# Performance work log

Measured on AMD Instinct MI355X. Metric: run time of the kernel, lower is better.

Reference implementation:

```python
import jax, jax.numpy as jnp
import numpy as np

B, N, C, H = 32, 577, 768, 12

def setup_inputs() -> dict:
    key = jax.random.key(0)
    k1, k2, k3, k4 = jax.random.split(key, 4)
    x = jax.random.normal(k1, (B, N, C), dtype=jnp.float32)
    prev = jax.random.normal(k2, (B, H, N, N), dtype=jnp.float32)
    Wqkv = jax.random.normal(k3, (3 * C, C), dtype=jnp.float32) * (C ** -0.5)
    Wproj = jax.random.normal(k4, (C, C), dtype=jnp.float32) * (C ** -0.5)
    bproj = jnp.zeros((C,), dtype=jnp.float32)
    return {"x": x, "prev": prev, "Wqkv": Wqkv, "Wproj": Wproj, "bproj": bproj}

def reference(x, prev, Wqkv, Wproj, bproj):
    b, n, c = x.shape
    h = H
    hd = c // h
    scale = hd ** -0.5
    # qkv: [B, N, 3C] -> [3, B, H, N, hd]
    qkv = (x @ Wqkv.T).reshape(b, n, 3, h, hd).transpose(2, 0, 3, 1, 4)
    q, k, v = qkv[0], qkv[1], qkv[2]
    # pre-softmax scores with residual passthrough (res_score=True)
    scores = jnp.einsum('bhqd,bhkd->bhqk', q, k) * scale + prev
    attn = jax.nn.softmax(scores, axis=-1)
    out = jnp.einsum('bhqk,bhkd->bhqd', attn, v)  # [B, H, N, hd]
    out = out.transpose(0, 2, 1, 3).reshape(b, n, c)
    out = out @ Wproj.T + bproj
    return out, scores
```

## Files before the change

kernel.cpp:

```cpp
#include <hip/hip_runtime.h>
#include <cstdint>
#include <cstddef>

using short8   = __attribute__((ext_vector_type(8))) short;
using f32x4    = __attribute__((ext_vector_type(4))) float;
using ushort4v = __attribute__((ext_vector_type(4))) unsigned short;

#define B_    32
#define N_    577
#define C_    768
#define H_    12
#define HD_   64
#define NPAD  640
#define MROWS 18464
#define MPAD  18560
#define NQKV  2304
#define SCALE 0.125f
#define OUT0_ELTS 14180352

static __device__ __forceinline__ unsigned short f2bf(float f) {
  union { float f; unsigned int u; } v; v.f = f;
  return (unsigned short)((v.u + 0x7FFFu + ((v.u >> 16) & 1u)) >> 16);
}

static __device__ __forceinline__ void gload_lds16(const unsigned short* g, unsigned short* l) {
  __builtin_amdgcn_global_load_lds(
      (const __attribute__((address_space(1))) unsigned int*)g,
      (__attribute__((address_space(3))) unsigned int*)l, 16, 0, 0);
}

__global__ __launch_bounds__(256) void cvt_f32_bf16(const float* __restrict__ src,
                                                    unsigned short* __restrict__ dst, int n4) {
  int i = blockIdx.x * 256 + threadIdx.x;
  if (i >= n4) return;
  f32x4 v = ((const f32x4*)src)[i];
  ushort4v o;
  o.x = f2bf(v.x); o.y = f2bf(v.y); o.z = f2bf(v.z); o.w = f2bf(v.w);
  ((ushort4v*)dst)[i] = o;
}

__global__ __launch_bounds__(256) void gemm_qkv(
    const unsigned short* __restrict__ A,
    const unsigned short* __restrict__ Bw,
    unsigned short* __restrict__ qb,
    unsigned short* __restrict__ kbuf,
    unsigned short* __restrict__ vtb)
{
  __shared__ union {
    struct { unsigned short A[128 * 64]; unsigned short B[128 * 64]; } st;
    unsigned short ct[128 * 128];
  } lds;
  const int mt = blockIdx.x, nt = blockIdx.y;
  const int tid = threadIdx.x;
  const int wave = tid >> 6, lane = tid & 63;
  const int wm = wave >> 1, wn = wave & 1;
  const int lq = lane & 15, grp = lane >> 4;

  f32x4 acc[4][4] = {};

  const int arowbase = mt * 128;
  const int browbase = nt * 128;
  const int srow = wave * 8 + (lane >> 3);
  const int scol = (lane & 7) * 8;

  for (int kblk = 0; kblk < 12; ++kblk) {
    const int koff = kblk * 64;
#pragma unroll
    for (int i = 0; i < 4; ++i) {
      gload_lds16(A  + (size_t)(arowbase + i * 32 + srow) * 768 + koff + scol,
                  &lds.st.A[(i * 32 + wave * 8) * 64]);
      gload_lds16(Bw + (size_t)(browbase + i * 32 + srow) * 768 + koff + scol,
                  &lds.st.B[(i * 32 + wave * 8) * 64]);
    }
    __syncthreads();
#pragma unroll
    for (int ks = 0; ks < 2; ++ks) {
      short8 af[4], bf[4];
#pragma unroll
      for (int mi = 0; mi < 4; ++mi)
        af[mi] = *(const short8*)&lds.st.A[(wm * 64 + mi * 16 + lq) * 64 + ks * 32 + grp * 8];
#pragma unroll
      for (int ni = 0; ni < 4; ++ni)
        bf[ni] = *(const short8*)&lds.st.B[(wn * 64 + ni * 16 + lq) * 64 + ks * 32 + grp * 8];
#pragma unroll
      for (int mi = 0; mi < 4; ++mi)
#pragma unroll
        for (int ni = 0; ni < 4; ++ni)
          acc[mi][ni] = __builtin_amdgcn_mfma_f32_16x16x32_bf16(af[mi], bf[ni], acc[mi][ni], 0, 0, 0);
    }
    __syncthreads();
  }

  const int s = nt / 6;

  if (s < 2) {
#pragma unroll
    for (int mi = 0; mi < 4; ++mi)
#pragma unroll
      for (int ni = 0; ni < 4; ++ni) {
        const int col = wn * 64 + ni * 16 + lq;
#pragma unroll
        for (int j = 0; j < 4; ++j) {
          const int row = wm * 64 + mi * 16 + grp * 4 + j;
          const int slot = (col >> 3) ^ (row & 7);
          lds.ct[row * 128 + slot * 8 + (col & 7)] = f2bf(acc[mi][ni][j]);
        }
      }
    __syncthreads();
    unsigned short* dstbase = (s == 0) ? qb : kbuf;
    const int h0 = (nt - s * 6) * 2;
#pragma unroll
    for (int p = 0; p < 4; ++p) {
      const int r  = p * 32 + (tid >> 3);
      const int cp = tid & 7;
      const int m  = arowbase + r;
      const unsigned bb = (unsigned)m / 577u;
      const int t = m - (int)bb * 577;
      const bool valid = (m < MROWS);
      const int cpos = cp ^ (t & 7);
#pragma unroll
      for (int hh = 0; hh < 2; ++hh) {
        const int slot = ((hh * 8 + cp) ^ (r & 7));
        short8 val = *(const short8*)&lds.ct[r * 128 + slot * 8];
        if (valid) {
          unsigned short* dst = dstbase +
              (((size_t)(bb * H_ + h0 + hh) * NPAD + t) * HD_ + cpos * 8);
          *(short8*)dst = val;
        }
      }
    }
  } else {
#pragma unroll
    for (int mi = 0; mi < 4; ++mi) {
#pragma unroll
      for (int ni = 0; ni < 4; ++ni) {
        const int n = browbase + wn * 64 + ni * 16 + lq;
        const int rem = n - 1536;
        const int hh = rem >> 6, d = rem & 63;
#pragma unroll
        for (int j = 0; j < 4; ++j) {
          const int m = arowbase + wm * 64 + mi * 16 + grp * 4 + j;
          if (m < MROWS) {
            const unsigned bb = (unsigned)m / 577u;
            const int t = m - (int)bb * 577;
            const int tloc = t & 63;
            const int newcol = (t & ~63) + ((((tloc >> 3) ^ (d & 7)) << 3)) + (t & 7);
            vtb[((size_t)bb * H_ + hh) * HD_ * NPAD + (size_t)d * NPAD + newcol] =
                f2bf(acc[mi][ni][j]);
          }
        }
      }
    }
  }
}

__global__ __launch_bounds__(256, 3) void attn_kernel(
    const unsigned short* __restrict__ qb,
    const unsigned short* __restrict__ kb,
    const unsigned short* __restrict__ vtb,
    const float* __restrict__ prev,
    float* __restrict__ scores_out,
    unsigned short* __restrict__ ob)
{
  const int qblk = blockIdx.x;
  const int bh   = blockIdx.y;
  const int tid  = threadIdx.x;
  const int wave = tid >> 6;
  const int lane = tid & 63;
  const int lq = lane & 15, grp = lane >> 4;

  const int b = bh / H_;
  const int h = bh - b * H_;

  const unsigned short* qp = qb  + (size_t)bh * NPAD * HD_;
  const unsigned short* kp = kb  + (size_t)bh * NPAD * HD_;
  const unsigned short* vp = vtb + (size_t)bh * HD_ * NPAD;

  const int qrow = qblk * 64 + wave * 16 + lq;
  const bool qvalid = (qrow < N_);
  const bool counted = (qblk < 9);

  const float* prevrow_c = prev + ((size_t)bh * N_ + (qvalid ? qrow : (N_ - 1))) * N_;
  const float* prevbh = prev + (size_t)bh * N_ * N_;
  float* srow_base = scores_out + (size_t)bh * N_ * N_;

  __shared__ __attribute__((aligned(16))) unsigned short ldsK[2][4096];
  __shared__ __attribute__((aligned(16))) unsigned short ldsV[2][4096];
  __shared__ __attribute__((aligned(16))) float sslab[4][16][68];

  short8 qf0, qf1;
  {
    const unsigned short* qr = qp + (size_t)qrow * HD_;
    qf0 = *(const short8*)(qr + ((grp)     ^ (lq & 7)) * 8);
    qf1 = *(const short8*)(qr + ((grp + 4) ^ (lq & 7)) * 8);
  }

  f32x4 oacc[4] = {};
  float lacc = 0.f;

  const int srow8 = wave * 8 + (lane >> 3);
  const int scol8 = (lane & 7) * 8;
  auto stageKV = [&](int kblk, int bufi) {
    const int kbase = kblk * 64;
#pragma unroll
    for (int r = 0; r < 2; ++r) {
      gload_lds16(kp + (size_t)(kbase + r * 32 + srow8) * HD_ + scol8,
                  &ldsK[bufi][r * 2048 + wave * 512]);
      gload_lds16(vp + (size_t)(r * 32 + srow8) * NPAD + kbase + scol8,
                  &ldsV[bufi][r * 2048 + wave * 512]);
    }
  };

  const int rl16  = lane >> 4;
  const int col0l = (lane & 15) * 4;
  int roff[4];
#pragma unroll
  for (int q4 = 0; q4 < 4; ++q4) {
    int r = qblk * 64 + wave * 16 + q4 * 4 + rl16;
    if (r >= N_) r = N_ - 1;
    roff[q4] = r * N_;
  }
  auto loadPrevC = [&](int kblk, f32x4 pv[4]) {
#pragma unroll
    for (int q4 = 0; q4 < 4; ++q4) {
      float tmp[4];
      __builtin_memcpy(tmp, prevbh + roff[q4] + kblk * 64 + col0l, 16);
      pv[q4][0] = tmp[0]; pv[q4][1] = tmp[1]; pv[q4][2] = tmp[2]; pv[q4][3] = tmp[3];
    }
  };

  const int sl0 = ((grp)     ^ (lq & 7)) * 8;
  const int sl1 = ((grp + 4) ^ (lq & 7)) * 8;

  f32x4 pvc[4], pvnc[4];
  stageKV(0, 0);
  asm volatile("" ::: "memory");
  loadPrevC(0, pvc);
  asm volatile("" ::: "memory");
  if (counted) asm volatile("s_waitcnt vmcnt(4)" ::: "memory");
  else         asm volatile("s_waitcnt vmcnt(0)" ::: "memory");
  __builtin_amdgcn_s_barrier();
  __builtin_amdgcn_sched_barrier(0);

#pragma unroll 1
  for (int kblk = 0; kblk < 9; ++kblk) {
    const int cur = kblk & 1;
    const int kbase = kblk * 64;

    stageKV(kblk + 1, cur ^ 1);
    asm volatile("" ::: "memory");
    if (kblk < 8) loadPrevC(kblk + 1, pvnc);
    asm volatile("" ::: "memory");

    f32x4 sacc[4] = {};
#pragma unroll
    for (int t = 0; t < 4; ++t) {
      const int row = (t * 16 + lq) * 64;
      short8 a0 = *(const short8*)&ldsK[cur][row + sl0];
      short8 a1 = *(const short8*)&ldsK[cur][row + sl1];
      sacc[t] = __builtin_amdgcn_mfma_f32_16x16x32_bf16(a0, qf0, sacc[t], 0, 0, 0);
      sacc[t] = __builtin_amdgcn_mfma_f32_16x16x32_bf16(a1, qf1, sacc[t], 0, 0, 0);
    }

#pragma unroll
    for (int t = 0; t < 4; ++t) {
      f32x4 sv;
#pragma unroll
      for (int r = 0; r < 4; ++r)
        sv[r] = sacc[t][r] * SCALE;
      *(f32x4*)&sslab[wave][lq][t * 16 + grp * 4] = sv;
    }

#pragma unroll
    for (int q4 = 0; q4 < 4; ++q4) {
      const int row16 = q4 * 4 + rl16;
      const int qrow_s = qblk * 64 + wave * 16 + row16;
      f32x4 vals = *(const f32x4*)&sslab[wave][row16][col0l];
      vals += pvc[q4];
      if (qrow_s < N_)
        __builtin_memcpy(srow_base + (size_t)qrow_s * N_ + kbase + col0l, &vals, 16);
      *(f32x4*)&sslab[wave][row16][col0l] = vals;
    }

    short8 pf0, pf1;
    {
      const float* sr = &sslab[wave][lq][0];
      f32x4 x0 = *(const f32x4*)(sr + grp * 8);
      f32x4 x1 = *(const f32x4*)(sr + grp * 8 + 4);
      f32x4 x2 = *(const f32x4*)(sr + 32 + grp * 8);
      f32x4 x3 = *(const f32x4*)(sr + 32 + grp * 8 + 4);
      float e[16];
#pragma unroll
      for (int j = 0; j < 4; ++j) {
        e[j]      = __expf(x0[j]);
        e[4 + j]  = __expf(x1[j]);
        e[8 + j]  = __expf(x2[j]);
        e[12 + j] = __expf(x3[j]);
      }
#pragma unroll
      for (int j = 0; j < 16; ++j) lacc += e[j];
      ushort4v pa, pb2, pc, pd;
#pragma unroll
      for (int j = 0; j < 4; ++j) {
        ((unsigned short*)&pa)[j]  = f2bf(e[j]);
        ((unsigned short*)&pb2)[j] = f2bf(e[4 + j]);
        ((unsigned short*)&pc)[j]  = f2bf(e[8 + j]);
        ((unsigned short*)&pd)[j]  = f2bf(e[12 + j]);
      }
      union { struct { ushort4v a, b; } s; short8 v; } u0, u1;
      u0.s.a = pa; u0.s.b = pb2; pf0 = u0.v;
      u1.s.a = pc; u1.s.b = pd;  pf1 = u1.v;
    }

#pragma unroll
    for (int dt = 0; dt < 4; ++dt) {
      const int row = (dt * 16 + lq) * 64;
      short8 v0 = *(const short8*)&ldsV[cur][row + sl0];
      short8 v1 = *(const short8*)&ldsV[cur][row + sl1];
      oacc[dt] = __builtin_amdgcn_mfma_f32_16x16x32_bf16(v0, pf0, oacc[dt], 0, 0, 0);
      oacc[dt] = __builtin_amdgcn_mfma_f32_16x16x32_bf16(v1, pf1, oacc[dt], 0, 0, 0);
    }

    if (counted) {
      if (kblk == 8) asm volatile("s_waitcnt vmcnt(4)" ::: "memory");
      else           asm volatile("s_waitcnt vmcnt(8)" ::: "memory");
    } else {
      asm volatile("s_waitcnt vmcnt(0)" ::: "memory");
    }
    __builtin_amdgcn_s_barrier();
    __builtin_amdgcn_sched_barrier(0);
#pragma unroll
    for (int i = 0; i < 4; ++i) pvc[i] = pvnc[i];
  }

  {
    f32x4 s0 = {};
    {
      const int row = lq * 64;
      short8 a0 = *(const short8*)&ldsK[1][row + sl0];
      short8 a1 = *(const short8*)&ldsK[1][row + sl1];
      s0 = __builtin_amdgcn_mfma_f32_16x16x32_bf16(a0, qf0, s0, 0, 0, 0);
      s0 = __builtin_amdgcn_mfma_f32_16x16x32_bf16(a1, qf1, s0, 0, 0, 0);
    }
    const float sval9 = s0[0] * SCALE + prevrow_c[576];
    const float e9 = (grp == 0) ? __expf(sval9) : 0.f;
    lacc += e9;
    short8 pf0 = {};
    ((unsigned short*)&pf0)[0] = f2bf(e9);
#pragma unroll
    for (int dt = 0; dt < 4; ++dt) {
      const int row = (dt * 16 + lq) * 64;
      short8 v0 = *(const short8*)&ldsV[1][row + sl0];
      oacc[dt] = __builtin_amdgcn_mfma_f32_16x16x32_bf16(v0, pf0, oacc[dt], 0, 0, 0);
    }
    if (grp == 0 && qvalid)
      srow_base[(size_t)qrow * N_ + 576] = sval9;
  }

  lacc += __shfl_xor(lacc, 16, 64);
  lacc += __shfl_xor(lacc, 32, 64);

  if (qvalid) {
    const float rl = 1.0f / lacc;
    unsigned short* orow = ob + (size_t)(b * N_ + qrow) * C_ + h * HD_;
#pragma unroll
    for (int dt = 0; dt < 4; ++dt) {
      ushort4v ow;
      ow.x = f2bf(oacc[dt][0] * rl); ow.y = f2bf(oacc[dt][1] * rl);
      ow.z = f2bf(oacc[dt][2] * rl); ow.w = f2bf(oacc[dt][3] * rl);
      *(ushort4v*)(orow + dt * 16 + grp * 4) = ow;
    }
  }
}

__global__ __launch_bounds__(256) void gemm_proj(
    const unsigned short* __restrict__ A,
    const unsigned short* __restrict__ Bw,
    const float* __restrict__ bias,
    float* __restrict__ out0)
{
  __shared__ unsigned short As[128 * 64];
  __shared__ unsigned short Bs[128 * 64];
  const int mt = blockIdx.x, nt = blockIdx.y;
  const int tid = threadIdx.x;
  const int wave = tid >> 6, lane = tid & 63;
  const int wm = wave >> 1, wn = wave & 1;
  const int lq = lane & 15, grp = lane >> 4;

  f32x4 acc[4][4] = {};

  const int arowbase = mt * 128;
  const int browbase = nt * 128;
  const int srow = wave * 8 + (lane >> 3);
  const int scol = (lane & 7) * 8;

  for (int kblk = 0; kblk < 12; ++kblk) {
    const int koff = kblk * 64;
#pragma unroll
    for (int i = 0; i < 4; ++i) {
      gload_lds16(A  + (size_t)(arowbase + i * 32 + srow) * 768 + koff + scol,
                  &As[(i * 32 + wave * 8) * 64]);
      gload_lds16(Bw + (size_t)(browbase + i * 32 + srow) * 768 + koff + scol,
                  &Bs[(i * 32 + wave * 8) * 64]);
    }
    __syncthreads();
#pragma unroll
    for (int ks = 0; ks < 2; ++ks) {
      short8 af[4], bf[4];
#pragma unroll
      for (int mi = 0; mi < 4; ++mi)
        af[mi] = *(const short8*)&As[(wm * 64 + mi * 16 + lq) * 64 + ks * 32 + grp * 8];
#pragma unroll
      for (int ni = 0; ni < 4; ++ni)
        bf[ni] = *(const short8*)&Bs[(wn * 64 + ni * 16 + lq) * 64 + ks * 32 + grp * 8];
#pragma unroll
      for (int mi = 0; mi < 4; ++mi)
#pragma unroll
        for (int ni = 0; ni < 4; ++ni)
          acc[mi][ni] = __builtin_amdgcn_mfma_f32_16x16x32_bf16(af[mi], bf[ni], acc[mi][ni], 0, 0, 0);
    }
    __syncthreads();
  }

#pragma unroll
  for (int ni = 0; ni < 4; ++ni) {
    const int n = browbase + wn * 64 + ni * 16 + lq;
    const float bv = bias[n];
#pragma unroll
    for (int mi = 0; mi < 4; ++mi) {
#pragma unroll
      for (int j = 0; j < 4; ++j) {
        const int m = arowbase + wm * 64 + mi * 16 + grp * 4 + j;
        if (m < MROWS) out0[(size_t)m * C_ + n] = acc[mi][ni][j] + bv;
      }
    }
  }
}

extern "C" void kernel_launch(void* const* d_in, const int* in_sizes, int n_in,
                              void* d_out, int out_size, void* d_ws, size_t ws_size,
                              hipStream_t stream) {
  const float* x     = (const float*)d_in[0];
  const float* prev  = (const float*)d_in[1];
  const float* Wqkv  = (const float*)d_in[2];
  const float* Wproj = (const float*)d_in[3];
  const float* bproj = (const float*)d_in[4];
  float* out = (float*)d_out;

  char* ws = (char*)d_ws;
  size_t off = 0;
  auto alloc = [&](size_t bytes) {
    void* p = ws + off;
    off += (bytes + 255) & ~(size_t)255;
    return p;
  };
  unsigned short* xb     = (unsigned short*)alloc((size_t)MPAD * 768 * 2);
  unsigned short* wqkvb  = (unsigned short*)alloc((size_t)NQKV * 768 * 2);
  unsigned short* wprojb = (unsigned short*)alloc((size_t)768 * 768 * 2);
  unsigned short* qb     = (unsigned short*)alloc((size_t)B_ * H_ * NPAD * HD_ * 2);
  unsigned short* kbuf   = (unsigned short*)alloc((size_t)B_ * H_ * NPAD * HD_ * 2);
  unsigned short* vtb    = (unsigned short*)alloc((size_t)B_ * H_ * HD_ * NPAD * 2);
  unsigned short* ob     = (unsigned short*)alloc((size_t)MPAD * 768 * 2);
  (void)ob;

  hipMemsetAsync(vtb, 0, (size_t)B_ * H_ * HD_ * NPAD * 2, stream);

  {
    int n4 = (B_ * N_ * C_) / 4;
    cvt_f32_bf16<<<(n4 + 255) / 256, 256, 0, stream>>>(x, xb, n4);
    n4 = (NQKV * C_) / 4;
    cvt_f32_bf16<<<(n4 + 255) / 256, 256, 0, stream>>>(Wqkv, wqkvb, n4);
    n4 = (C_ * C_) / 4;
    cvt_f32_bf16<<<(n4 + 255) / 256, 256, 0, stream>>>(Wproj, wprojb, n4);
  }

  gemm_qkv<<<dim3(MPAD / 128, NQKV / 128), 256, 0, stream>>>(xb, wqkvb, qb, kbuf, vtb);

  attn_kernel<<<dim3(10, B_ * H_), 256, 0, stream>>>(qb, kbuf, vtb, prev,
                                                     out + OUT0_ELTS, ob);

  gemm_proj<<<dim3(MPAD / 128, C_ / 128), 256, 0, stream>>>(ob, wprojb, bproj, out);
}
```

Measured before the change: 580.9 us.

## Merge conversion kernels, zero only V tail, stage proj output via LDS

Folds the three fp32-to-bf16 conversion launches into one kernel that picks its source by thread index. The full memset of the transposed V buffer becomes a small kernel that zeroes only the padded tail columns 576..639. The projection GEMM epilogue now stages accumulators in XOR-swizzled LDS and writes coalesced float4 rows, replacing scattered scalar stores. This cuts launch count and memset traffic and improves store coalescing, at the cost of extra barriers in the epilogue.

```diff
diff --git a/kernel.cpp b/kernel.cpp
--- a/kernel.cpp
+++ b/kernel.cpp
@@ -29,14 +29,29 @@
       (__attribute__((address_space(3))) unsigned int*)l, 16, 0, 0);
 }
 
-__global__ __launch_bounds__(256) void cvt_f32_bf16(const float* __restrict__ src,
-                                                    unsigned short* __restrict__ dst, int n4) {
-  int i = blockIdx.x * 256 + threadIdx.x;
-  if (i >= n4) return;
-  f32x4 v = ((const f32x4*)src)[i];
+__global__ __launch_bounds__(256) void cvt_all(
+    const float* __restrict__ x, const float* __restrict__ wqkv,
+    const float* __restrict__ wproj,
+    unsigned short* __restrict__ xb, unsigned short* __restrict__ wqkvb,
+    unsigned short* __restrict__ wprojb) {
+  const int i = blockIdx.x * 256 + threadIdx.x;
+  const int n1 = (B_ * N_ * C_) / 4;
+  const int n2 = n1 + (NQKV * C_) / 4;
+  const float* src; unsigned short* dst; int j;
+  if (i < n1)      { src = x;     dst = xb;     j = i; }
+  else if (i < n2) { src = wqkv;  dst = wqkvb;  j = i - n1; }
+  else             { src = wproj; dst = wprojb; j = i - n2; }
+  f32x4 v = ((const f32x4*)src)[j];
   ushort4v o;
   o.x = f2bf(v.x); o.y = f2bf(v.y); o.z = f2bf(v.z); o.w = f2bf(v.w);
-  ((ushort4v*)dst)[i] = o;
+  ((ushort4v*)dst)[j] = o;
+}
+
+__global__ __launch_bounds__(256) void zero_vtb_tail(unsigned short* __restrict__ vtb) {
+  const int i = blockIdx.x * 256 + threadIdx.x;
+  const int row = i >> 3, c = i & 7;
+  short8 z = {};
+  *(short8*)(vtb + (size_t)row * NPAD + 576 + c * 8) = z;
 }
 
 __global__ __launch_bounds__(256) void gemm_qkv(
@@ -379,8 +394,10 @@
     const float* __restrict__ bias,
     float* __restrict__ out0)
 {
-  __shared__ unsigned short As[128 * 64];
-  __shared__ unsigned short Bs[128 * 64];
+  __shared__ union {
+    struct { unsigned short A[128 * 64]; unsigned short B[128 * 64]; } st;
+    float ct32[128 * 64];
+  } lds;
   const int mt = blockIdx.x, nt = blockIdx.y;
   const int tid = threadIdx.x;
   const int wave = tid >> 6, lane = tid & 63;
@@ -399,9 +416,9 @@
 #pragma unroll
     for (int i = 0; i < 4; ++i) {
       gload_lds16(A  + (size_t)(arowbase + i * 32 + srow) * 768 + koff + scol,
-                  &As[(i * 32 + wave * 8) * 64]);
+                  &lds.st.A[(i * 32 + wave * 8) * 64]);
       gload_lds16(Bw + (size_t)(browbase + i * 32 + srow) * 768 + koff + scol,
-                  &Bs[(i * 32 + wave * 8) * 64]);
+                  &lds.st.B[(i * 32 + wave * 8) * 64]);
     }
     __syncthreads();
 #pragma unroll
@@ -409,10 +426,10 @@
       short8 af[4], bf[4];
 #pragma unroll
       for (int mi = 0; mi < 4; ++mi)
-        af[mi] = *(const short8*)&As[(wm * 64 + mi * 16 + lq) * 64 + ks * 32 + grp * 8];
+        af[mi] = *(const short8*)&lds.st.A[(wm * 64 + mi * 16 + lq) * 64 + ks * 32 + grp * 8];
 #pragma unroll
       for (int ni = 0; ni < 4; ++ni)
-        bf[ni] = *(const short8*)&Bs[(wn * 64 + ni * 16 + lq) * 64 + ks * 32 + grp * 8];
+        bf[ni] = *(const short8*)&lds.st.B[(wn * 64 + ni * 16 + lq) * 64 + ks * 32 + grp * 8];
 #pragma unroll
       for (int mi = 0; mi < 4; ++mi)
 #pragma unroll
@@ -423,16 +440,32 @@
   }
 
 #pragma unroll
-  for (int ni = 0; ni < 4; ++ni) {
-    const int n = browbase + wn * 64 + ni * 16 + lq;
-    const float bv = bias[n];
-#pragma unroll
-    for (int mi = 0; mi < 4; ++mi) {
-#pragma unroll
-      for (int j = 0; j < 4; ++j) {
-        const int m = arowbase + wm * 64 + mi * 16 + grp * 4 + j;
-        if (m < MROWS) out0[(size_t)m * C_ + n] = acc[mi][ni][j] + bv;
+  for (int hh2 = 0; hh2 < 2; ++hh2) {
+    __syncthreads();
+    if (wn == hh2) {
+#pragma unroll
+      for (int ni = 0; ni < 4; ++ni) {
+        const int colh = ni * 16 + lq;
+        const int cc = colh >> 2, el = colh & 3;
+        const float bv = bias[browbase + hh2 * 64 + colh];
+#pragma unroll
+        for (int mi = 0; mi < 4; ++mi)
+#pragma unroll
+          for (int j = 0; j < 4; ++j) {
+            const int row = wm * 64 + mi * 16 + grp * 4 + j;
+            lds.ct32[row * 64 + ((cc ^ (row & 7)) << 2) + el] = acc[mi][ni][j] + bv;
+          }
       }
+    }
+    __syncthreads();
+#pragma unroll
+    for (int p = 0; p < 8; ++p) {
+      const int row = p * 16 + wave * 4 + (lane >> 4);
+      const int cc = lane & 15;
+      const int m = arowbase + row;
+      f32x4 val = *(const f32x4*)&lds.ct32[row * 64 + ((cc ^ (row & 7)) << 2)];
+      if (m < MROWS)
+        *(f32x4*)&out0[(size_t)m * C_ + browbase + hh2 * 64 + cc * 4] = val;
     }
   }
 }
@@ -463,16 +496,9 @@
   unsigned short* ob     = (unsigned short*)alloc((size_t)MPAD * 768 * 2);
   (void)ob;
 
-  hipMemsetAsync(vtb, 0, (size_t)B_ * H_ * HD_ * NPAD * 2, stream);
-
-  {
-    int n4 = (B_ * N_ * C_) / 4;
-    cvt_f32_bf16<<<(n4 + 255) / 256, 256, 0, stream>>>(x, xb, n4);
-    n4 = (NQKV * C_) / 4;
-    cvt_f32_bf16<<<(n4 + 255) / 256, 256, 0, stream>>>(Wqkv, wqkvb, n4);
-    n4 = (C_ * C_) / 4;
-    cvt_f32_bf16<<<(n4 + 255) / 256, 256, 0, stream>>>(Wproj, wprojb, n4);
-  }
+  zero_vtb_tail<<<768, 256, 0, stream>>>(vtb);
+
+  cvt_all<<<16152, 256, 0, stream>>>(x, Wqkv, Wproj, xb, wqkvb, wprojb);
 
   gemm_qkv<<<dim3(MPAD / 128, NQKV / 128), 256, 0, stream>>>(xb, wqkvb, qb, kbuf, vtb);
 
```

Result: slower. 698.2 us (+20.2%).
